# Optimization experiments

Hardware: AMD Instinct MI355X
Metric: run time of the kernel (lower is better)

## Reference

```python
import jax, jax.numpy as jnp
import numpy as np

NUM_HEADS = 8
NUM_LEVELS = 4
NUM_POINTS = 4
EMBED_DIM = 256
HEAD_DIM = EMBED_DIM // NUM_HEADS  # 32
SUM_POINTS = NUM_LEVELS * NUM_POINTS  # 16
OFFSET_SCALE = 0.5
SPATIAL = [(80, 80), (40, 40), (20, 20), (10, 10)]


def _bilinear_gather(v_flat, x, y, H, W):
    """grid_sample(bilinear, padding zeros, align_corners=False) via gathers.
    v_flat: (BN, c, H*W); x, y: (BN, Lq, P) pixel coords. -> (BN, c, Lq*P)"""
    BN = v_flat.shape[0]
    x0 = jnp.floor(x)
    y0 = jnp.floor(y)
    wx1 = x - x0
    wy1 = y - y0

    def corner(xi, yi, w):
        valid = (xi >= 0) & (xi <= W - 1) & (yi >= 0) & (yi <= H - 1)
        xc = jnp.clip(xi, 0, W - 1).astype(jnp.int32)
        yc = jnp.clip(yi, 0, H - 1).astype(jnp.int32)
        idx = (yc * W + xc).reshape(BN, -1)  # (BN, Lq*P)
        g = jnp.take_along_axis(v_flat, idx[:, None, :], axis=2)  # (BN, c, Lq*P)
        return g * (w * valid).reshape(BN, 1, -1)

    return (corner(x0, y0, (1.0 - wx1) * (1.0 - wy1))
            + corner(x0 + 1.0, y0, wx1 * (1.0 - wy1))
            + corner(x0, y0 + 1.0, (1.0 - wx1) * wy1)
            + corner(x0 + 1.0, y0 + 1.0, wx1 * wy1))


def setup_inputs() -> dict:
    key = jax.random.key(0)
    ks = jax.random.split(key, 6)
    bs, Lq = 16, 300
    spatial = np.array(SPATIAL, dtype=np.int64)
    Lv = int((spatial[:, 0] * spatial[:, 1]).sum())  # 8500

    query = jax.random.normal(ks[0], (bs, Lq, EMBED_DIM), jnp.float32)
    reference_points = jax.random.uniform(ks[1], (bs, Lq, 1, 4), jnp.float32)  # cx,cy,w,h in (0,1)
    value = jax.random.normal(ks[2], (bs, NUM_HEADS, HEAD_DIM, Lv), jnp.float32)

    W_off = jax.random.normal(ks[3], (EMBED_DIM, NUM_HEADS * SUM_POINTS * 2), jnp.float32) * 0.01
    # bias from _reset_parameters grid init
    thetas = np.arange(NUM_HEADS, dtype=np.float32) * (2.0 * np.pi / NUM_HEADS)
    grid = np.stack([np.cos(thetas), np.sin(thetas)], -1)
    grid = grid / np.abs(grid).max(-1, keepdims=True)
    grid = np.tile(grid.reshape(NUM_HEADS, 1, 2), (1, SUM_POINTS, 1))
    scaling = np.concatenate([np.arange(1, NUM_POINTS + 1) for _ in range(NUM_LEVELS)]).reshape(1, -1, 1)
    b_off = jnp.asarray((grid * scaling).reshape(-1), jnp.float32)

    W_attn = jax.random.normal(ks[4], (EMBED_DIM, NUM_HEADS * SUM_POINTS), jnp.float32) * 0.01
    b_attn = jnp.zeros((NUM_HEADS * SUM_POINTS,), jnp.float32)
    num_points_scale = jnp.full((SUM_POINTS,), 1.0 / NUM_POINTS, jnp.float32)

    return {"query": query, "reference_points": reference_points, "value": value,
            "value_spatial_shapes": spatial, "W_off": W_off, "b_off": b_off,
            "W_attn": W_attn, "b_attn": b_attn, "num_points_scale": num_points_scale}


def reference(query, reference_points, value, value_spatial_shapes,
              W_off, b_off, W_attn, b_attn, num_points_scale):
    bs, Lq, _ = query.shape
    BN = bs * NUM_HEADS

    off = (query @ W_off + b_off).reshape(bs, Lq, NUM_HEADS, SUM_POINTS, 2)
    attn = jax.nn.softmax((query @ W_attn + b_attn).reshape(bs, Lq, NUM_HEADS, SUM_POINTS), axis=-1)

    # box branch: reference_points (bs, Lq, 1, 4); [..., 2:] = wh scales offsets
    offset = off * num_points_scale[:, None] * reference_points[:, :, None, :, 2:] * OFFSET_SCALE
    loc = reference_points[:, :, None, :, :2] + offset  # (bs, Lq, H, SUM_POINTS, 2) in [0,1]

    grids = 2.0 * loc - 1.0
    grids = jnp.transpose(grids, (0, 2, 1, 3, 4)).reshape(BN, Lq, SUM_POINTS, 2)
    attn = jnp.transpose(attn, (0, 2, 1, 3)).reshape(BN, 1, Lq, SUM_POINTS)

    shapes = np.asarray(value_spatial_shapes)
    lvl_sizes = (shapes[:, 0] * shapes[:, 1]).tolist()
    v_levels = jnp.split(value.reshape(BN, HEAD_DIM, -1), np.cumsum(lvl_sizes)[:-1], axis=2)
    g_levels = jnp.split(grids, np.arange(NUM_POINTS, SUM_POINTS, NUM_POINTS), axis=2)

    sampled = []
    for (H, W), v_l, g_l in zip(shapes.tolist(), v_levels, g_levels):
        # align_corners=False pixel coords
        x = (g_l[..., 0] + 1.0) * (W * 0.5) - 0.5
        y = (g_l[..., 1] + 1.0) * (H * 0.5) - 0.5
        s = _bilinear_gather(v_l, x, y, H, W).reshape(BN, HEAD_DIM, Lq, NUM_POINTS)
        sampled.append(s)
    sampled = jnp.concatenate(sampled, axis=-1)  # (BN, c, Lq, SUM_POINTS)

    out = (sampled * attn).sum(-1)  # (BN, c, Lq)
    out = out.reshape(bs, NUM_HEADS * HEAD_DIM, Lq).transpose(0, 2, 1)  # (bs, Lq, embed_dim)
    return out
```

## Files before the change

### kernel.cpp

```cpp
#include <hip/hip_runtime.h>
#include <hip/hip_bf16.h>
#include <math.h>

#define BS 16
#define LQ 300
#define NH 8
#define HD 32
#define SP 16
#define ED 256
#define LV 8500
#define NB_BLK 300
#define PXT 256
#define TR_PER_BN 34
#define NTR_BLK (TR_PER_BN * 128)
#define TSTR 264

static __device__ __forceinline__ int imin(int a, int b) { return a < b ? a : b; }
static __device__ __forceinline__ int imax(int a, int b) { return a > b ? a : b; }

static __device__ __forceinline__ unsigned short f2bf(float x) {
    unsigned u = __float_as_uint(x);
    unsigned r = (u + 0x7fffu + ((u >> 16) & 1u)) >> 16;
    return (unsigned short)r;
}

__global__ __launch_bounds__(256) void kF(const float* __restrict__ query,
                                          const float* __restrict__ refp,
                                          const float* __restrict__ Woff,
                                          const float* __restrict__ boff,
                                          const float* __restrict__ Wattn,
                                          const float* __restrict__ battn,
                                          const float* __restrict__ nps,
                                          float* __restrict__ la,
                                          const float* __restrict__ v,
                                          __hip_bfloat16* __restrict__ vt,
                                          int nb) {
    __shared__ float s[32 * TSTR];
    const int tid = threadIdx.x;

    if ((int)blockIdx.x >= nb) {
        const int t   = blockIdx.x - nb;
        const int bn  = t / TR_PER_BN;
        const int px0 = (t - bn * TR_PER_BN) * PXT;
        const int nlv = imin(PXT, LV - px0);

        const int w   = tid >> 6;
        const int px4 = (tid & 63) * 4;
        const float* src = v + (size_t)bn * (HD * LV) + px0 + px4;
        float4 r[8];
        if (px4 < nlv) {
#pragma unroll
            for (int k = 0; k < 8; ++k) {
                int row = w + 4 * k;
                r[k] = *reinterpret_cast<const float4*>(src + (size_t)row * LV);
            }
#pragma unroll
            for (int k = 0; k < 8; ++k) {
                int row = w + 4 * k;
                *reinterpret_cast<float4*>(s + row * TSTR + px4) = r[k];
            }
        }
        __syncthreads();
        const int p2 = tid >> 2;
        const int q  = tid & 3;
        char* dst0 = (char*)vt + ((size_t)bn * LV + px0) * (HD * 2) + q * 16;
#pragma unroll
        for (int j = 0; j < 4; ++j) {
            int p = p2 + 64 * j;
            if (p < nlv) {
                unsigned pk[4];
#pragma unroll
                for (int i = 0; i < 4; ++i) {
                    float f0 = s[(8 * q + 2 * i) * TSTR + p];
                    float f1 = s[(8 * q + 2 * i + 1) * TSTR + p];
                    pk[i] = (unsigned)f2bf(f0) | ((unsigned)f2bf(f1) << 16);
                }
                *reinterpret_cast<uint4*>(dst0 + (size_t)p * 64) =
                    make_uint4(pk[0], pk[1], pk[2], pk[3]);
            }
        }
        return;
    }

    float* qbuf = s;
    float* lbuf = s;
    const int gq0 = blockIdx.x * 16;

    const float* qsrc = query + (size_t)gq0 * ED;
#pragma unroll
    for (int i = 0; i < 16; ++i) qbuf[tid + 256 * i] = qsrc[tid + 256 * i];
    __syncthreads();

    const int qi = tid >> 5;
    const int cl = tid & 31;
    const float* qa = qbuf + qi * ED;
    const float* qb = qbuf + (qi + 8) * ED;

    float a0[4] = {0,0,0,0}, a1[4] = {0,0,0,0}, a2[4] = {0,0,0,0};
    float c0[4] = {0,0,0,0}, c1[4] = {0,0,0,0}, c2[4] = {0,0,0,0};
    const float4* w0 = (const float4*)(Woff + cl * 4);
    const float4* w1 = (const float4*)(Woff + 128 + cl * 4);
    const float4* w2 = (const float4*)(Wattn + cl * 4);
#pragma unroll 4
    for (int k = 0; k < ED; ++k) {
        float va = qa[k], vb = qb[k];
        float4 x0 = w0[k * 64];
        float4 x1 = w1[k * 64];
        float4 x2 = w2[k * 32];
        a0[0] += va * x0.x; a0[1] += va * x0.y; a0[2] += va * x0.z; a0[3] += va * x0.w;
        a1[0] += va * x1.x; a1[1] += va * x1.y; a1[2] += va * x1.z; a1[3] += va * x1.w;
        a2[0] += va * x2.x; a2[1] += va * x2.y; a2[2] += va * x2.z; a2[3] += va * x2.w;
        c0[0] += vb * x0.x; c0[1] += vb * x0.y; c0[2] += vb * x0.z; c0[3] += vb * x0.w;
        c1[0] += vb * x1.x; c1[1] += vb * x1.y; c1[2] += vb * x1.z; c1[3] += vb * x1.w;
        c2[0] += vb * x2.x; c2[1] += vb * x2.y; c2[2] += vb * x2.z; c2[3] += vb * x2.w;
    }
    __syncthreads();
    {
        float* ra = lbuf + qi * 384;
        float* rb = lbuf + (qi + 8) * 384;
#pragma unroll
        for (int u = 0; u < 4; ++u) {
            float bo0 = boff[cl * 4 + u];
            float bo1 = boff[128 + cl * 4 + u];
            float ba  = battn[cl * 4 + u];
            ra[cl * 4 + u]       = a0[u] + bo0;
            ra[128 + cl * 4 + u] = a1[u] + bo1;
            ra[256 + cl * 4 + u] = a2[u] + ba;
            rb[cl * 4 + u]       = c0[u] + bo0;
            rb[128 + cl * 4 + u] = c1[u] + bo1;
            rb[256 + cl * 4 + u] = c2[u] + ba;
        }
    }
    __syncthreads();

#pragma unroll
    for (int it = 0; it < 2; ++it) {
        const int slot = it * 256 + tid;
        const int qi2 = slot >> 5;
        const int h2  = (slot >> 2) & 7;
        const int pg  = slot & 3;
        const float* lr = lbuf + qi2 * 384;

        float l[4];
#pragma unroll
        for (int i = 0; i < 4; ++i) l[i] = lr[256 + h2 * 16 + pg * 4 + i];
        float m = fmaxf(fmaxf(l[0], l[1]), fmaxf(l[2], l[3]));
        m = fmaxf(m, __shfl_xor(m, 1));
        m = fmaxf(m, __shfl_xor(m, 2));
        float e[4];
        float ps = 0.f;
#pragma unroll
        for (int i = 0; i < 4; ++i) { e[i] = expf(l[i] - m); ps += e[i]; }
        ps += __shfl_xor(ps, 1);
        ps += __shfl_xor(ps, 2);
        float inv = 1.f / ps;

        const int gq = gq0 + qi2;
        const int b  = gq / LQ;
        const int q  = gq - b * LQ;
        const float* rp = refp + (size_t)gq * 4;
        float cx = rp[0], cy = rp[1], rw = rp[2], rh = rp[3];

        const int Wl = 80 >> pg;
        const int base = (25600 - (25600 >> (2 * pg))) / 3;
        const float fw = (float)Wl;

        float* dst = la + ((((size_t)b * NH + h2) * LQ + q) * SP + pg * 4) * 8;
#pragma unroll
        for (int i = 0; i < 4; ++i) {
            int p = pg * 4 + i;
            float ox = lr[h2 * 32 + p * 2 + 0];
            float oy = lr[h2 * 32 + p * 2 + 1];
            float sc = nps[p] * 0.5f;
            float locx = cx + ox * sc * rw;
            float locy = cy + oy * sc * rh;
            float x = locx * fw - 0.5f;
            float y = locy * fw - 0.5f;
            float aw = e[i] * inv;

            float x0f = floorf(x), y0f = floorf(y);
            float fx = x - x0f, fy = y - y0f;
            int ix0 = (int)x0f, iy0 = (int)y0f;
            int ix1 = ix0 + 1, iy1 = iy0 + 1;
            bool vx0 = (ix0 >= 0) && (ix0 < Wl);
            bool vx1 = (ix1 >= 0) && (ix1 < Wl);
            bool vy0 = (iy0 >= 0) && (iy0 < Wl);
            bool vy1 = (iy1 >= 0) && (iy1 < Wl);
            int cx0 = imin(imax(ix0, 0), Wl - 1);
            int cx1 = imin(imax(ix1, 0), Wl - 1);
            int cy0 = imin(imax(iy0, 0), Wl - 1);
            int cy1 = imin(imax(iy1, 0), Wl - 1);
            float w00 = aw * (1.f - fx) * (1.f - fy) * ((vx0 && vy0) ? 1.f : 0.f);
            float w10 = aw * fx * (1.f - fy) * ((vx1 && vy0) ? 1.f : 0.f);
            float w01 = aw * (1.f - fx) * fy * ((vx0 && vy1) ? 1.f : 0.f);
            float w11 = aw * fx * fy * ((vx1 && vy1) ? 1.f : 0.f);
            int i00 = base + cy0 * Wl + cx0;
            int i10 = base + cy0 * Wl + cx1;
            int i01 = base + cy1 * Wl + cx0;
            int i11 = base + cy1 * Wl + cx1;

            *reinterpret_cast<float4*>(dst + i * 8) = make_float4(w00, w10, w01, w11);
            *reinterpret_cast<int4*>(dst + i * 8 + 4) = make_int4(i00, i10, i01, i11);
        }
    }
}

__global__ __launch_bounds__(128) void kC4(const __hip_bfloat16* __restrict__ vt,
                                           const float* __restrict__ la,
                                           float* __restrict__ out) {
    const int bid = blockIdx.x;
    const int logical = (bid & 7) * 160 + (bid >> 3);
    const int bh = logical / 10;
    const int qt = logical - bh * 10;
    const int b = bh >> 3;
    const int h = bh & 7;

    const int tid = threadIdx.x;
    const int qs = tid >> 2;
    const int l4 = tid & 3;
    const int q = qt * 32 + qs;
    if (q >= LQ) return;

    const float* lq = la + ((size_t)bh * LQ + q) * (SP * 8);
    const char* vb = (const char*)vt + (size_t)bh * LV * (HD * 2) + l4 * 16;

    float acc[8] = {0.f, 0.f, 0.f, 0.f, 0.f, 0.f, 0.f, 0.f};

#pragma unroll 2
    for (int p = 0; p < SP; p += 2) {
        float4 wv0 = *reinterpret_cast<const float4*>(lq + p * 8);
        int4  iv0  = *reinterpret_cast<const int4*>(lq + p * 8 + 4);
        float4 wv1 = *reinterpret_cast<const float4*>(lq + p * 8 + 8);
        int4  iv1  = *reinterpret_cast<const int4*>(lq + p * 8 + 12);
        uint4 r0 = *reinterpret_cast<const uint4*>(vb + (size_t)iv0.x * 64);
        uint4 r1 = *reinterpret_cast<const uint4*>(vb + (size_t)iv0.y * 64);
        uint4 r2 = *reinterpret_cast<const uint4*>(vb + (size_t)iv0.z * 64);
        uint4 r3 = *reinterpret_cast<const uint4*>(vb + (size_t)iv0.w * 64);
        uint4 r4 = *reinterpret_cast<const uint4*>(vb + (size_t)iv1.x * 64);
        uint4 r5 = *reinterpret_cast<const uint4*>(vb + (size_t)iv1.y * 64);
        uint4 r6 = *reinterpret_cast<const uint4*>(vb + (size_t)iv1.z * 64);
        uint4 r7 = *reinterpret_cast<const uint4*>(vb + (size_t)iv1.w * 64);
#define FMA8(W, R)                                                             \
        {                                                                      \
            union { unsigned u; float f; } _t;                                 \
            _t.u = (R).x << 16;         acc[0] = fmaf((W), _t.f, acc[0]);      \
            _t.u = (R).x & 0xffff0000u; acc[1] = fmaf((W), _t.f, acc[1]);      \
            _t.u = (R).y << 16;         acc[2] = fmaf((W), _t.f, acc[2]);      \
            _t.u = (R).y & 0xffff0000u; acc[3] = fmaf((W), _t.f, acc[3]);      \
            _t.u = (R).z << 16;         acc[4] = fmaf((W), _t.f, acc[4]);      \
            _t.u = (R).z & 0xffff0000u; acc[5] = fmaf((W), _t.f, acc[5]);      \
            _t.u = (R).w << 16;         acc[6] = fmaf((W), _t.f, acc[6]);      \
            _t.u = (R).w & 0xffff0000u; acc[7] = fmaf((W), _t.f, acc[7]);      \
        }
        FMA8(wv0.x, r0) FMA8(wv0.y, r1) FMA8(wv0.z, r2) FMA8(wv0.w, r3)
        FMA8(wv1.x, r4) FMA8(wv1.y, r5) FMA8(wv1.z, r6) FMA8(wv1.w, r7)
#undef FMA8
    }
    float* op = out + ((size_t)b * LQ + q) * ED + h * HD + l4 * 8;
    *reinterpret_cast<float4*>(op)     = make_float4(acc[0], acc[1], acc[2], acc[3]);
    *reinterpret_cast<float4*>(op + 4) = make_float4(acc[4], acc[5], acc[6], acc[7]);
}

__global__ __launch_bounds__(320) void kCfb(const float* __restrict__ val,
                                            const float* __restrict__ la,
                                            float* __restrict__ out) {
    __shared__ __align__(16) float sla[10 * SP * 8];
    int bid = blockIdx.x;
    int logical = (bid & 7) * 480 + (bid >> 3);
    int bh = logical / 30;
    int qt = logical - bh * 30;
    int b = bh >> 3;
    int h = bh & 7;
    const int tid = threadIdx.x;
    const float* lsrc = la + (((size_t)bh * LQ + qt * 10) * SP) * 8;
    for (int i = tid; i < 1280; i += 320) sla[i] = lsrc[i];
    __syncthreads();
    const int qs = tid >> 5;
    const int c  = tid & 31;
    const float* vb = val + ((size_t)bh * HD + c) * LV;
    float acc = 0.f;
    const float* lq = sla + qs * (SP * 8);
#pragma unroll
    for (int p = 0; p < SP; ++p) {
        float4 wv = *reinterpret_cast<const float4*>(lq + p * 8);
        int4  iv  = *reinterpret_cast<const int4*>(lq + p * 8 + 4);
        acc += wv.x * vb[iv.x];
        acc += wv.y * vb[iv.y];
        acc += wv.z * vb[iv.z];
        acc += wv.w * vb[iv.w];
    }
    int q = qt * 10 + qs;
    out[((size_t)b * LQ + q) * ED + h * HD + c] = acc;
}

extern "C" void kernel_launch(void* const* d_in, const int* in_sizes, int n_in,
                              void* d_out, int out_size, void* d_ws, size_t ws_size,
                              hipStream_t stream) {
    const float* query = (const float*)d_in[0];
    const float* refp  = (const float*)d_in[1];
    const float* value = (const float*)d_in[2];
    const float* Woff  = (const float*)d_in[4];
    const float* boff  = (const float*)d_in[5];
    const float* Wattn = (const float*)d_in[6];
    const float* battn = (const float*)d_in[7];
    const float* nps   = (const float*)d_in[8];
    float* out = (float*)d_out;

    const size_t la_bytes = (size_t)BS * NH * LQ * SP * 8 * sizeof(float);
    const size_t vt_bytes = (size_t)BS * NH * LV * HD * sizeof(__hip_bfloat16);
    float* la = (float*)d_ws;
    __hip_bfloat16* vt = (__hip_bfloat16*)((char*)d_ws + la_bytes);
    const bool use_tr = ws_size >= la_bytes + vt_bytes;

    if (use_tr) {
        kF<<<dim3(NB_BLK + NTR_BLK), 256, 0, stream>>>(query, refp, Woff, boff,
                                                       Wattn, battn, nps, la,
                                                       value, vt, NB_BLK);
        kC4<<<dim3(1280), 128, 0, stream>>>(vt, la, out);
    } else {
        kF<<<dim3(NB_BLK), 256, 0, stream>>>(query, refp, Woff, boff,
                                             Wattn, battn, nps, la,
                                             value, (__hip_bfloat16*)nullptr, NB_BLK);
        kCfb<<<dim3(3840), 320, 0, stream>>>(value, la, out);
    }
}
```

Measured before the change: 76.28 us.

## Convert to bf16 before LDS staging and reorder sampling-table layout

The value-transpose path now converts fp32 to bf16 right after the global load and stores packed bf16 pairs in shared memory with an odd stride, which halves LDS footprint and traffic and avoids bank conflicts. The read side unpacks halves according to pixel parity. The location/weight table is reordered from (b,h,q) to (b,q,h) so that the producer writes contiguously per query across heads. Both consumer kernels are updated to match the new indexing. The cost is extra shift and mask work in the transpose, and a strided table read for the kC4 consumer.

```diff
diff --git a/kernel.cpp b/kernel.cpp
--- a/kernel.cpp
+++ b/kernel.cpp
@@ -13,15 +13,14 @@
 #define PXT 256
 #define TR_PER_BN 34
 #define NTR_BLK (TR_PER_BN * 128)
-#define TSTR 264
+#define TSTR2 129
 
 static __device__ __forceinline__ int imin(int a, int b) { return a < b ? a : b; }
 static __device__ __forceinline__ int imax(int a, int b) { return a > b ? a : b; }
 
-static __device__ __forceinline__ unsigned short f2bf(float x) {
+static __device__ __forceinline__ unsigned f2bf(float x) {
     unsigned u = __float_as_uint(x);
-    unsigned r = (u + 0x7fffu + ((u >> 16) & 1u)) >> 16;
-    return (unsigned short)r;
+    return (u + 0x7fffu + ((u >> 16) & 1u)) >> 16;
 }
 
 __global__ __launch_bounds__(256) void kF(const float* __restrict__ query,
@@ -35,10 +34,11 @@
                                           const float* __restrict__ v,
                                           __hip_bfloat16* __restrict__ vt,
                                           int nb) {
-    __shared__ float s[32 * TSTR];
+    __shared__ float s[16 * 384];
     const int tid = threadIdx.x;
 
     if ((int)blockIdx.x >= nb) {
+        unsigned* su = reinterpret_cast<unsigned*>(s);
         const int t   = blockIdx.x - nb;
         const int bn  = t / TR_PER_BN;
         const int px0 = (t - bn * TR_PER_BN) * PXT;
@@ -47,17 +47,17 @@
         const int w   = tid >> 6;
         const int px4 = (tid & 63) * 4;
         const float* src = v + (size_t)bn * (HD * LV) + px0 + px4;
-        float4 r[8];
         if (px4 < nlv) {
+            float4 r[8];
+#pragma unroll
+            for (int k = 0; k < 8; ++k)
+                r[k] = *reinterpret_cast<const float4*>(src + (size_t)(w + 4 * k) * LV);
 #pragma unroll
             for (int k = 0; k < 8; ++k) {
-                int row = w + 4 * k;
-                r[k] = *reinterpret_cast<const float4*>(src + (size_t)row * LV);
-            }
-#pragma unroll
-            for (int k = 0; k < 8; ++k) {
-                int row = w + 4 * k;
-                *reinterpret_cast<float4*>(s + row * TSTR + px4) = r[k];
+                unsigned lo = f2bf(r[k].x) | (f2bf(r[k].y) << 16);
+                unsigned hi = f2bf(r[k].z) | (f2bf(r[k].w) << 16);
+                *reinterpret_cast<uint2*>(su + (w + 4 * k) * TSTR2 + (px4 >> 1)) =
+                    make_uint2(lo, hi);
             }
         }
         __syncthreads();
@@ -68,12 +68,15 @@
         for (int j = 0; j < 4; ++j) {
             int p = p2 + 64 * j;
             if (p < nlv) {
+                int col = p >> 1;
+                int odd = p & 1;
                 unsigned pk[4];
 #pragma unroll
                 for (int i = 0; i < 4; ++i) {
-                    float f0 = s[(8 * q + 2 * i) * TSTR + p];
-                    float f1 = s[(8 * q + 2 * i + 1) * TSTR + p];
-                    pk[i] = (unsigned)f2bf(f0) | ((unsigned)f2bf(f1) << 16);
+                    unsigned u0 = su[(8 * q + 2 * i) * TSTR2 + col];
+                    unsigned u1 = su[(8 * q + 2 * i + 1) * TSTR2 + col];
+                    pk[i] = odd ? ((u0 >> 16) | (u1 & 0xffff0000u))
+                                : ((u0 & 0xffffu) | (u1 << 16));
                 }
                 *reinterpret_cast<uint4*>(dst0 + (size_t)p * 64) =
                     make_uint4(pk[0], pk[1], pk[2], pk[3]);
@@ -165,7 +168,7 @@
         const int base = (25600 - (25600 >> (2 * pg))) / 3;
         const float fw = (float)Wl;
 
-        float* dst = la + ((((size_t)b * NH + h2) * LQ + q) * SP + pg * 4) * 8;
+        float* dst = la + ((((size_t)b * LQ + q) * NH + h2) * SP + pg * 4) * 8;
 #pragma unroll
         for (int i = 0; i < 4; ++i) {
             int p = pg * 4 + i;
@@ -221,7 +224,7 @@
     const int q = qt * 32 + qs;
     if (q >= LQ) return;
 
-    const float* lq = la + ((size_t)bh * LQ + q) * (SP * 8);
+    const float* lq = la + (((size_t)b * LQ + q) * NH + h) * (SP * 8);
     const char* vb = (const char*)vt + (size_t)bh * LV * (HD * 2) + l4 * 16;
 
     float acc[8] = {0.f, 0.f, 0.f, 0.f, 0.f, 0.f, 0.f, 0.f};
@@ -272,8 +275,11 @@
     int b = bh >> 3;
     int h = bh & 7;
     const int tid = threadIdx.x;
-    const float* lsrc = la + (((size_t)bh * LQ + qt * 10) * SP) * 8;
-    for (int i = tid; i < 1280; i += 320) sla[i] = lsrc[i];
+    const int q0 = qt * 10;
+    for (int i = tid; i < 1280; i += 320) {
+        int qq = i >> 7, j = i & 127;
+        sla[i] = la[(((size_t)b * LQ + q0 + qq) * NH + h) * 128 + j];
+    }
     __syncthreads();
     const int qs = tid >> 5;
     const int c  = tid & 31;
@@ -289,7 +295,7 @@
         acc += wv.z * vb[iv.z];
         acc += wv.w * vb[iv.w];
     }
-    int q = qt * 10 + qs;
+    int q = q0 + qs;
     out[((size_t)b * LQ + q) * ED + h * HD + c] = acc;
 }
 
```

Measured after the change: 95.44 us. 25.1% more time.
